# Performance work log

Hardware: AMD Instinct MI355X
Metric: run time of the kernel (lower is better)

## Reference

```python
import math
import jax, jax.numpy as jnp
import numpy as np

NUM_HEADS = 4
HEAD_DIM = 384


def reshape_fortran(x, shape):
    # column-major (Fortran) reshape, matching the torch reverse-permute trick
    x = jnp.transpose(x, tuple(reversed(range(x.ndim))))
    x = x.reshape(tuple(reversed(shape)))
    return jnp.transpose(x, tuple(reversed(range(len(shape)))))


def rel_pos_rotate(data):
    # data: [b, n_heads, L=2M-1, S] -> [b, n_heads, S, S]
    data = jnp.transpose(data, (0, 2, 3, 1))  # [b, d0=L, d1=S, d2=H]
    b, d0, d1, d2 = data.shape
    data = jnp.concatenate([data, jnp.zeros((b, d1, d1, d2), data.dtype)], axis=1)
    data = reshape_fortran(data, (b, (d0 + d1) * d1, 1, d2))
    data = data[:, :(d1 + d0 - 1) * d1]
    data = reshape_fortran(data, (b, d0 + d1 - 1, d1, d2))
    n = d0 // 2
    data = jnp.swapaxes(data[:, n:n + d1], 1, 2)  # [b, d1, d1, d2]
    return jnp.transpose(data, (0, 3, 1, 2))      # [b, H, S, S]


def setup_inputs() -> dict:
    key = jax.random.key(0)
    ks = jax.random.split(key, 5)
    B, S, D = 4, 920, 1536
    M = 920
    return {
        "hidden_states": jax.random.normal(ks[0], (B, S, D), jnp.float32),
        "q_w": jax.random.normal(ks[1], (D, NUM_HEADS * HEAD_DIM), jnp.float32) * 0.02,
        "k_w": jax.random.normal(ks[2], (D, NUM_HEADS * HEAD_DIM), jnp.float32) * 0.02,
        "v_w": jax.random.normal(ks[3], (D, NUM_HEADS * HEAD_DIM), jnp.float32) * 0.02,
        "dist_emb": jax.random.normal(ks[4], (2 * M - 1, HEAD_DIM), jnp.float32) * 0.02,
    }


def reference(hidden_states, q_w, k_w, v_w, dist_emb):
    B, S, D = hidden_states.shape

    def heads(x):  # [B,S,H*hd] -> [B,H,S,hd]
        return jnp.transpose(x.reshape(B, S, NUM_HEADS, HEAD_DIM), (0, 2, 1, 3))

    # query is pre-scaled by 1/sqrt(head_dim), matching the torch code
    q = heads((hidden_states @ q_w) / math.sqrt(HEAD_DIM))
    k = heads(hidden_states @ k_w)
    v = heads(hidden_states @ v_w)

    scores = jnp.einsum("bhqd,bhkd->bhqk", q, k)  # [B,H,S,S]
    # relative position scores: [B,H,L,S] then skew-rotated into [B,H,S,S]
    rel = jnp.einsum("ld,bhsd->bhls", dist_emb, q)
    scores = scores + rel_pos_rotate(rel)

    probs = jax.nn.softmax(scores, axis=-1)
    ctx = jnp.einsum("bhqk,bhkd->bhqd", probs, v)  # [B,H,S,hd]
    ctx = jnp.transpose(ctx, (0, 2, 1, 3)).reshape(B, S, NUM_HEADS * HEAD_DIM)
    return ctx
```

## Files before the change

kernel.cpp:

```cpp
#include <hip/hip_runtime.h>
#include <cstdint>
#include <cstddef>

#define SEQ   920
#define DM    1536
#define DH    384
#define NHD   4
#define NB    4
#define NBH   16
#define MTOK  3680
#define NREL  1839

typedef short          bf16x8 __attribute__((ext_vector_type(8)));
typedef float          f32x4  __attribute__((ext_vector_type(4)));
typedef unsigned short u16x4  __attribute__((ext_vector_type(4)));
typedef unsigned short u16x8  __attribute__((ext_vector_type(8)));

__device__ __forceinline__ unsigned short f2bf(float f){
  union{float f; unsigned u;} v; v.f = f;
  unsigned r = v.u + 0x7FFFu + ((v.u >> 16) & 1u);
  return (unsigned short)(r >> 16);
}
__device__ __forceinline__ float bf2f(unsigned short h){
  union{unsigned u; float f;} v; v.u = ((unsigned)h) << 16;
  return v.f;
}
__device__ __forceinline__ f32x4 mfma_bf16(bf16x8 a, bf16x8 b, f32x4 c){
  return __builtin_amdgcn_mfma_f32_16x16x32_bf16(a, b, c, 0, 0, 0);
}
__device__ __forceinline__ void gload_lds16(const void* g, void* l){
  __builtin_amdgcn_global_load_lds((const __attribute__((address_space(1))) void*)g,
                                   (__attribute__((address_space(3))) void*)l, 16, 0, 0);
}

__global__ __launch_bounds__(256) void k_f2bf(const float* __restrict__ src,
                                              unsigned short* __restrict__ dst, int n){
  int i = (blockIdx.x * 256 + threadIdx.x) * 4;
  int stride = gridDim.x * 256 * 4;
  for(; i + 3 < n; i += stride){
    f32x4 v = *(const f32x4*)(src + i);
    u16x4 o; o.x = f2bf(v.x); o.y = f2bf(v.y); o.z = f2bf(v.z); o.w = f2bf(v.w);
    *(u16x4*)(dst + i) = o;
  }
}

__global__ __launch_bounds__(256) void k_wt3(const float* __restrict__ qw,
                                             const float* __restrict__ kw,
                                             const float* __restrict__ vw,
                                             unsigned short* __restrict__ wt){
  __shared__ float t[32][33];
  const float* w = blockIdx.z == 0 ? qw : (blockIdx.z == 1 ? kw : vw);
  int k0 = blockIdx.x * 32, n0 = blockIdx.y * 32;
  int tx = threadIdx.x, ty = threadIdx.y;
  #pragma unroll
  for(int j = 0; j < 4; j++)
    t[ty*4+j][tx] = w[(size_t)(k0 + ty*4 + j) * DM + n0 + tx];
  __syncthreads();
  #pragma unroll
  for(int j = 0; j < 4; j++)
    wt[(size_t)(blockIdx.z*DM + n0 + ty*4 + j) * DM + k0 + tx] = f2bf(t[tx][ty*4+j]);
}

template<class Epi>
__device__ __forceinline__ void gemm192(const unsigned short* __restrict__ A, int lda, int Amax,
                                        const unsigned short* __restrict__ B, int ldb, int Bmax,
                                        int K, int m0, int n0, Epi epi){
  __shared__ unsigned short As[3*192*64];
  __shared__ unsigned short Bs[3*192*64];
  const int tid = threadIdx.x;
  const int w = tid >> 6, l = tid & 63;
  const int lg = l >> 4, lo = l & 15;
  const int wm = w >> 2, wn = w & 3;

  const char* ga[3]; const char* gb[3];
  #pragma unroll
  for(int r = 0; r < 3; r++){
    int row = r*64 + (tid >> 3);
    int gslot = (tid & 7) ^ (row & 7);
    int ar = m0 + row; ar = ar < Amax ? ar : Amax - 1;
    ga[r] = (const char*)A + (size_t)ar*lda*2 + gslot*16;
    int br = n0 + row; br = br < Bmax ? br : Bmax - 1;
    gb[r] = (const char*)B + (size_t)br*ldb*2 + gslot*16;
  }
  const int ldst = tid * 16;

  auto stage = [&](int kt, int slot){
    size_t koff = (size_t)kt * 128;
    #pragma unroll
    for(int r = 0; r < 3; r++){
      gload_lds16(ga[r] + koff, (char*)As + slot*24576 + r*8192 + ldst);
      gload_lds16(gb[r] + koff, (char*)Bs + slot*24576 + r*8192 + ldst);
    }
  };

  f32x4 acc[6][3] = {};
  const int sw = (lo & 7) << 4;
  const int nk = (2*K + 127) >> 7;
  const int tb = 2*K - (nk - 1)*128;
  const bool keep0 = (lg*16) < tb;
  const bool keep1 = (64 + lg*16) < tb;

  auto compute = [&](int slot, bool last){
    const char* Ab = (const char*)As + slot*24576;
    const char* Bb = (const char*)Bs + slot*24576;
    bf16x8 af[6][2], bf[3][2];
    #pragma unroll
    for(int fi = 0; fi < 6; fi++){
      int row = wm*96 + fi*16 + lo;
      #pragma unroll
      for(int kk = 0; kk < 2; kk++)
        af[fi][kk] = *(const bf16x8*)(Ab + row*128 + ((kk*64 + lg*16) ^ sw));
    }
    #pragma unroll
    for(int fj = 0; fj < 3; fj++){
      int row = wn*48 + fj*16 + lo;
      #pragma unroll
      for(int kk = 0; kk < 2; kk++)
        bf[fj][kk] = *(const bf16x8*)(Bb + row*128 + ((kk*64 + lg*16) ^ sw));
    }
    if(last){
      #pragma unroll
      for(int fi = 0; fi < 6; fi++){
        if(!keep0) af[fi][0] = bf16x8{};
        if(!keep1) af[fi][1] = bf16x8{};
      }
    }
    __builtin_amdgcn_s_setprio(1);
    #pragma unroll
    for(int kk = 0; kk < 2; kk++)
      #pragma unroll
      for(int fi = 0; fi < 6; fi++)
        #pragma unroll
        for(int fj = 0; fj < 3; fj++)
          acc[fi][fj] = mfma_bf16(af[fi][kk], bf[fj][kk], acc[fi][fj]);
    __builtin_amdgcn_s_setprio(0);
  };

  stage(0, 0);
  stage(1, 1);
  int st = 0;
  for(int t = 0; t < nk; t++){
    if(t + 2 < nk){
      int s2 = st + 2 >= 3 ? st - 1 : st + 2;
      stage(t + 2, s2);
      asm volatile("s_waitcnt vmcnt(12)" ::: "memory");
    } else if(t + 1 < nk){
      asm volatile("s_waitcnt vmcnt(6)" ::: "memory");
    } else {
      asm volatile("s_waitcnt vmcnt(0)" ::: "memory");
    }
    __builtin_amdgcn_s_barrier();
    compute(st, t == nk - 1);
    __builtin_amdgcn_s_barrier();
    st = st + 1 >= 3 ? 0 : st + 1;
  }

  #pragma unroll
  for(int fi = 0; fi < 6; fi++)
    #pragma unroll
    for(int fj = 0; fj < 3; fj++){
      int m = m0 + wm*96 + fi*16 + lg*4;
      int n = n0 + wn*48 + fj*16 + lo;
      epi(m, n, acc[fi][fj]);
    }
}

__global__ __launch_bounds__(512) void k_proj(const unsigned short* __restrict__ X,
                                              const unsigned short* __restrict__ Wt,
                                              unsigned short* __restrict__ Qb,
                                              unsigned short* __restrict__ Kb,
                                              unsigned short* __restrict__ Vt){
  int bid = blockIdx.x;
  int wg  = (bid & 7) * 60 + (bid >> 3);
  int m0 = (wg % 20) * 192, n0 = (wg / 20) * 192;
  gemm192(X, DM, MTOK, Wt, DM, 3*DM, DM, m0, n0,
    [=] __device__ (int m, int n, f32x4 v4){
      if(m >= MTOK) return;
      int which = n / DM, r = n % DM, h = r / DH, d = r % DH;
      int b = m / SEQ, s = m % SEQ;
      int bh = b * NHD + h;
      if(which == 2){
        u16x4 o;
        o.x = f2bf(v4.x); o.y = f2bf(v4.y); o.z = f2bf(v4.z); o.w = f2bf(v4.w);
        *(u16x4*)(Vt + ((size_t)bh*DH + d)*SEQ + s) = o;
      } else if(which == 0){
        #pragma unroll
        for(int i = 0; i < 4; i++)
          Qb[((size_t)bh*SEQ + s + i)*DH + d] = f2bf(v4[i] * 0.05103103630798287f);
      } else {
        #pragma unroll
        for(int i = 0; i < 4; i++)
          Kb[((size_t)bh*SEQ + s + i)*DH + d] = f2bf(v4[i]);
      }
    });
}

__global__ __launch_bounds__(512) void k_rel(const unsigned short* __restrict__ Qb,
                                             const unsigned short* __restrict__ E,
                                             unsigned short* __restrict__ relS){
  int m0 = blockIdx.x * 192, n0 = blockIdx.y * 192;
  int s0 = m0 % SEQ;
  int qlo = s0, qhi = s0 + 191;
  if(qhi >= SEQ){ qlo = 0; qhi = SEQ - 1; }
  if(n0 + 191 < 919 - qhi || n0 > 1838 - qlo) return;
  gemm192(Qb, DH, NBH*SEQ, E, DH, NREL, DH, m0, n0,
    [=] __device__ (int m, int n, f32x4 v4){
      #pragma unroll
      for(int i = 0; i < 4; i++){
        int mi = m + i;
        if(mi >= NBH*SEQ) continue;
        int q = mi % SEQ;
        int j = n - 919 + q;
        if(j < 0 || j >= SEQ) continue;
        relS[(size_t)mi*SEQ + j] = f2bf(v4[i]);
      }
    });
}

__global__ __launch_bounds__(512) void k_sgemm(const unsigned short* __restrict__ Qb,
                                               const unsigned short* __restrict__ Kb,
                                               unsigned short* __restrict__ P){
  int id = blockIdx.x;
  int idp = (id & 7) * 50 + (id >> 3);
  int bh = idp / 25, r = idp % 25;
  int m0 = (r % 5) * 192, n0 = (r / 5) * 192;
  const unsigned short* A = Qb + (size_t)bh*SEQ*DH;
  const unsigned short* B = Kb + (size_t)bh*SEQ*DH;
  unsigned short* Pbh = P + (size_t)bh*SEQ*SEQ;
  gemm192(A, DH, SEQ, B, DH, SEQ, DH, m0, n0,
    [=] __device__ (int m, int n, f32x4 v4){
      if(n >= SEQ) return;
      #pragma unroll
      for(int i = 0; i < 4; i++){
        int mi = m + i;
        if(mi >= SEQ) continue;
        size_t off = (size_t)mi*SEQ + n;
        float p = __expf(v4[i] + bf2f(Pbh[off]));
        Pbh[off] = f2bf(p);
      }
    });
}

__global__ __launch_bounds__(256) void k_rowsum(const unsigned short* __restrict__ P,
                                                float* __restrict__ rs){
  int w = threadIdx.x >> 6, l = threadIdx.x & 63;
  #pragma unroll
  for(int r = 0; r < 4; r++){
    int row = blockIdx.x * 16 + w * 4 + r;
    size_t base = (size_t)row * SEQ;
    float s = 0.f;
    for(int c = l; c < 115; c += 64){
      u16x8 v = *(const u16x8*)(P + base + (size_t)c*8);
      #pragma unroll
      for(int j = 0; j < 8; j++) s += bf2f(v[j]);
    }
    s += __shfl_xor(s, 1);  s += __shfl_xor(s, 2);  s += __shfl_xor(s, 4);
    s += __shfl_xor(s, 8);  s += __shfl_xor(s, 16); s += __shfl_xor(s, 32);
    if(l == 0) rs[row] = s;
  }
}

__global__ __launch_bounds__(512) void k_pv(const unsigned short* __restrict__ P,
                                            const unsigned short* __restrict__ Vt,
                                            const float* __restrict__ rs,
                                            float* __restrict__ out){
  int id = blockIdx.x;
  int idp = (id & 7) * 20 + (id >> 3);
  int bh = idp / 10, r = idp % 10;
  int m0 = (r % 5) * 192, n0 = (r / 5) * 192;
  const unsigned short* A = P  + (size_t)bh*SEQ*SEQ;
  const unsigned short* B = Vt + (size_t)bh*DH*SEQ;
  const float* rsb = rs + (size_t)bh*SEQ;
  const int b = bh >> 2, h = bh & 3;
  gemm192(A, SEQ, SEQ, B, SEQ, DH, SEQ, m0, n0,
    [=] __device__ (int m, int n, f32x4 v4){
      #pragma unroll
      for(int i = 0; i < 4; i++){
        int mi = m + i;
        if(mi >= SEQ) continue;
        out[((size_t)(b*SEQ + mi))*DM + h*DH + n] = v4[i] / rsb[mi];
      }
    });
}

extern "C" void kernel_launch(void* const* d_in, const int* in_sizes, int n_in,
                              void* d_out, int out_size, void* d_ws, size_t ws_size,
                              hipStream_t stream){
  const float* X  = (const float*)d_in[0];
  const float* qw = (const float*)d_in[1];
  const float* kw = (const float*)d_in[2];
  const float* vw = (const float*)d_in[3];
  const float* de = (const float*)d_in[4];
  float* out = (float*)d_out;
  char* ws = (char*)d_ws;

  unsigned short* Qb   = (unsigned short*)ws;
  unsigned short* Kb   = (unsigned short*)(ws + 11304960);
  unsigned short* Vt   = (unsigned short*)(ws + 22609920);
  unsigned short* relS = (unsigned short*)(ws + 33914880);
  unsigned short* Eb   = (unsigned short*)(ws + 60999680);
  unsigned short* Xb   = (unsigned short*)(ws + 33914880);
  unsigned short* Wt   = (unsigned short*)(ws + 45219840);
  float*          rsum = (float*)ws;

  k_f2bf<<<dim3(2048), dim3(256), 0, stream>>>(X,  Xb, MTOK*DM);
  k_f2bf<<<dim3(690),  dim3(256), 0, stream>>>(de, Eb, NREL*DH);
  k_wt3<<<dim3(48,48,3), dim3(32,8), 0, stream>>>(qw, kw, vw, Wt);
  k_proj<<<dim3(480), dim3(512), 0, stream>>>(Xb, Wt, Qb, Kb, Vt);
  k_rel<<<dim3(77,10), dim3(512), 0, stream>>>(Qb, Eb, relS);
  k_sgemm<<<dim3(400), dim3(512), 0, stream>>>(Qb, Kb, relS);
  k_rowsum<<<dim3(920), dim3(256), 0, stream>>>(relS, rsum);
  k_pv<<<dim3(160), dim3(512), 0, stream>>>(relS, Vt, rsum, out);
}
```

Before: 230.9 us.

## Interleave GEMM LDS fragment loads and prefetch with MFMA in three phases

Splits each K-tile's compute into three phases of two A-fragments each. Every phase issues one slice of the next-next tile's global-to-LDS prefetch, interleaved with LDS reads and MFMA blocks. The aim is to spread memory traffic across the iteration instead of issuing it all up front, and to lower register pressure from holding all A fragments. It adds extra barriers per iteration and changes the vmcnt wait pattern, which could cost more in synchronization than it saves.

After: 219.7 us. 4.9% less time.

```diff
diff --git a/kernel.cpp b/kernel.cpp
--- a/kernel.cpp
+++ b/kernel.cpp
@@ -84,13 +84,10 @@
   }
   const int ldst = tid * 16;
 
-  auto stage = [&](int kt, int slot){
+  auto stage_pair = [&](int kt, int slot, int r){
     size_t koff = (size_t)kt * 128;
-    #pragma unroll
-    for(int r = 0; r < 3; r++){
-      gload_lds16(ga[r] + koff, (char*)As + slot*24576 + r*8192 + ldst);
-      gload_lds16(gb[r] + koff, (char*)Bs + slot*24576 + r*8192 + ldst);
-    }
+    gload_lds16(ga[r] + koff, (char*)As + slot*24576 + r*8192 + ldst);
+    gload_lds16(gb[r] + koff, (char*)Bs + slot*24576 + r*8192 + ldst);
   };
 
   f32x4 acc[6][3] = {};
@@ -100,58 +97,119 @@
   const bool keep0 = (lg*16) < tb;
   const bool keep1 = (64 + lg*16) < tb;
 
-  auto compute = [&](int slot, bool last){
-    const char* Ab = (const char*)As + slot*24576;
-    const char* Bb = (const char*)Bs + slot*24576;
-    bf16x8 af[6][2], bf[3][2];
-    #pragma unroll
-    for(int fi = 0; fi < 6; fi++){
-      int row = wm*96 + fi*16 + lo;
-      #pragma unroll
-      for(int kk = 0; kk < 2; kk++)
-        af[fi][kk] = *(const bf16x8*)(Ab + row*128 + ((kk*64 + lg*16) ^ sw));
-    }
+  #pragma unroll
+  for(int r = 0; r < 3; r++) stage_pair(0, 0, r);
+  #pragma unroll
+  for(int r = 0; r < 3; r++) stage_pair(1, 1, r);
+  asm volatile("s_waitcnt vmcnt(6)" ::: "memory");
+  __builtin_amdgcn_s_barrier();
+
+  int st = 0;
+  for(int t = 0; t < nk; t++){
+    const bool last = (t == nk - 1);
+    const bool pf = (t + 2 < nk);
+    const int s2 = st + 2 >= 3 ? st - 1 : st + 2;
+    const char* Ab = (const char*)As + st*24576;
+    const char* Bb = (const char*)Bs + st*24576;
+
+    bf16x8 bfr[3][2], afr[2][2];
+
     #pragma unroll
     for(int fj = 0; fj < 3; fj++){
       int row = wn*48 + fj*16 + lo;
       #pragma unroll
       for(int kk = 0; kk < 2; kk++)
-        bf[fj][kk] = *(const bf16x8*)(Bb + row*128 + ((kk*64 + lg*16) ^ sw));
-    }
+        bfr[fj][kk] = *(const bf16x8*)(Bb + row*128 + ((kk*64 + lg*16) ^ sw));
+    }
+    #pragma unroll
+    for(int fi = 0; fi < 2; fi++){
+      int row = wm*96 + fi*16 + lo;
+      #pragma unroll
+      for(int kk = 0; kk < 2; kk++)
+        afr[fi][kk] = *(const bf16x8*)(Ab + row*128 + ((kk*64 + lg*16) ^ sw));
+    }
+    if(pf) stage_pair(t + 2, s2, 0);
     if(last){
       #pragma unroll
-      for(int fi = 0; fi < 6; fi++){
-        if(!keep0) af[fi][0] = bf16x8{};
-        if(!keep1) af[fi][1] = bf16x8{};
-      }
-    }
+      for(int fi = 0; fi < 2; fi++){
+        if(!keep0) afr[fi][0] = bf16x8{};
+        if(!keep1) afr[fi][1] = bf16x8{};
+      }
+    }
+    __builtin_amdgcn_s_barrier();
+    asm volatile("s_waitcnt lgkmcnt(0)" ::: "memory");
     __builtin_amdgcn_s_setprio(1);
     #pragma unroll
     for(int kk = 0; kk < 2; kk++)
       #pragma unroll
-      for(int fi = 0; fi < 6; fi++)
+      for(int fi = 0; fi < 2; fi++)
         #pragma unroll
         for(int fj = 0; fj < 3; fj++)
-          acc[fi][fj] = mfma_bf16(af[fi][kk], bf[fj][kk], acc[fi][fj]);
+          acc[fi][fj] = mfma_bf16(afr[fi][kk], bfr[fj][kk], acc[fi][fj]);
     __builtin_amdgcn_s_setprio(0);
-  };
-
-  stage(0, 0);
-  stage(1, 1);
-  int st = 0;
-  for(int t = 0; t < nk; t++){
-    if(t + 2 < nk){
-      int s2 = st + 2 >= 3 ? st - 1 : st + 2;
-      stage(t + 2, s2);
-      asm volatile("s_waitcnt vmcnt(12)" ::: "memory");
+    __builtin_amdgcn_s_barrier();
+
+    #pragma unroll
+    for(int fi = 0; fi < 2; fi++){
+      int row = wm*96 + (fi + 2)*16 + lo;
+      #pragma unroll
+      for(int kk = 0; kk < 2; kk++)
+        afr[fi][kk] = *(const bf16x8*)(Ab + row*128 + ((kk*64 + lg*16) ^ sw));
+    }
+    if(pf) stage_pair(t + 2, s2, 1);
+    if(last){
+      #pragma unroll
+      for(int fi = 0; fi < 2; fi++){
+        if(!keep0) afr[fi][0] = bf16x8{};
+        if(!keep1) afr[fi][1] = bf16x8{};
+      }
+    }
+    __builtin_amdgcn_s_barrier();
+    asm volatile("s_waitcnt lgkmcnt(0)" ::: "memory");
+    __builtin_amdgcn_s_setprio(1);
+    #pragma unroll
+    for(int kk = 0; kk < 2; kk++)
+      #pragma unroll
+      for(int fi = 0; fi < 2; fi++)
+        #pragma unroll
+        for(int fj = 0; fj < 3; fj++)
+          acc[fi + 2][fj] = mfma_bf16(afr[fi][kk], bfr[fj][kk], acc[fi + 2][fj]);
+    __builtin_amdgcn_s_setprio(0);
+    __builtin_amdgcn_s_barrier();
+
+    #pragma unroll
+    for(int fi = 0; fi < 2; fi++){
+      int row = wm*96 + (fi + 4)*16 + lo;
+      #pragma unroll
+      for(int kk = 0; kk < 2; kk++)
+        afr[fi][kk] = *(const bf16x8*)(Ab + row*128 + ((kk*64 + lg*16) ^ sw));
+    }
+    if(pf){
+      stage_pair(t + 2, s2, 2);
+      asm volatile("s_waitcnt vmcnt(6)" ::: "memory");
     } else if(t + 1 < nk){
-      asm volatile("s_waitcnt vmcnt(6)" ::: "memory");
-    } else {
       asm volatile("s_waitcnt vmcnt(0)" ::: "memory");
     }
-    __builtin_amdgcn_s_barrier();
-    compute(st, t == nk - 1);
-    __builtin_amdgcn_s_barrier();
+    if(last){
+      #pragma unroll
+      for(int fi = 0; fi < 2; fi++){
+        if(!keep0) afr[fi][0] = bf16x8{};
+        if(!keep1) afr[fi][1] = bf16x8{};
+      }
+    }
+    __builtin_amdgcn_s_barrier();
+    asm volatile("s_waitcnt lgkmcnt(0)" ::: "memory");
+    __builtin_amdgcn_s_setprio(1);
+    #pragma unroll
+    for(int kk = 0; kk < 2; kk++)
+      #pragma unroll
+      for(int fi = 0; fi < 2; fi++)
+        #pragma unroll
+        for(int fj = 0; fj < 3; fj++)
+          acc[fi + 4][fj] = mfma_bf16(afr[fi][kk], bfr[fj][kk], acc[fi + 4][fj]);
+    __builtin_amdgcn_s_setprio(0);
+    __builtin_amdgcn_s_barrier();
+
     st = st + 1 >= 3 ? 0 : st + 1;
   }
 
```

## Switch GEMMs to 128x128 tiles with B fragments loaded directly to registers

Applied to the files above, without the earlier changes.

Replaces the shared 192x192 GEMM core, which staged both operands through LDS, with a 128x128 core. Only A is staged through LDS, in a 4-deep ring. B fragments are read straight from global memory into double-buffered registers, which halves LDS traffic and cuts one barrier per k-step. Smaller tiles with launch_bounds(512,4) raise the block count and occupancy, and grids and XCD-aware block mappings are recomputed for every GEMM kernel. The cost is uncoalesced per-lane global reads for B, plus less data reuse per tile.

After: 288.5 us. +24.9%, slower.

```diff
diff --git a/kernel.cpp b/kernel.cpp
--- a/kernel.cpp
+++ b/kernel.cpp
@@ -61,119 +61,125 @@
     wt[(size_t)(blockIdx.z*DM + n0 + ty*4 + j) * DM + k0 + tx] = f2bf(t[tx][ty*4+j]);
 }
 
-template<class Epi>
-__device__ __forceinline__ void gemm192(const unsigned short* __restrict__ A, int lda, int Amax,
+#define GITER(T, BFC, BFN)                                                     \
+  {                                                                            \
+    const int t_ = (T);                                                        \
+    __builtin_amdgcn_s_barrier();                                              \
+    const char* Ab = (const char*)As + (t_ & 3)*16384;                         \
+    bf16x8 af[4][2];                                                           \
+    _Pragma("unroll")                                                          \
+    for(int fi = 0; fi < 4; fi++){                                             \
+      int row = wm*64 + fi*16 + lo;                                            \
+      _Pragma("unroll")                                                        \
+      for(int kk = 0; kk < 2; kk++)                                            \
+        af[fi][kk] = *(const bf16x8*)(Ab + row*128 + ((kk*64 + lg*16) ^ sw));  \
+    }                                                                          \
+    if(t_ + 1 < nk) loadB(t_ + 1, BFN);                                        \
+    if(t_ + 3 < nk) stageA(t_ + 3, (t_ + 3) & 3);                              \
+    if(t_ == nk - 1){                                                          \
+      _Pragma("unroll")                                                        \
+      for(int fi = 0; fi < 4; fi++){                                           \
+        if(!keep0) af[fi][0] = bf16x8{};                                       \
+        if(!keep1) af[fi][1] = bf16x8{};                                       \
+      }                                                                        \
+    }                                                                          \
+    __builtin_amdgcn_s_setprio(1);                                             \
+    _Pragma("unroll")                                                          \
+    for(int kk = 0; kk < 2; kk++)                                              \
+      _Pragma("unroll")                                                        \
+      for(int fi = 0; fi < 4; fi++)                                            \
+        _Pragma("unroll")                                                      \
+        for(int fj = 0; fj < 2; fj++)                                          \
+          acc[fi][fj] = mfma_bf16(af[fi][kk], BFC[fj][kk], acc[fi][fj]);       \
+    __builtin_amdgcn_s_setprio(0);                                             \
+    if(t_ + 2 < nk){ asm volatile("s_waitcnt vmcnt(2)" ::: "memory"); }        \
+    else           { asm volatile("s_waitcnt vmcnt(0)" ::: "memory"); }        \
+  }
+
+template<bool CLAMP_B, class Epi>
+__device__ __forceinline__ void gemm128(const unsigned short* __restrict__ A, int lda, int Amax,
                                         const unsigned short* __restrict__ B, int ldb, int Bmax,
                                         int K, int m0, int n0, Epi epi){
-  __shared__ unsigned short As[3*192*64];
-  __shared__ unsigned short Bs[3*192*64];
+  __shared__ unsigned short As[4*128*64];
   const int tid = threadIdx.x;
   const int w = tid >> 6, l = tid & 63;
   const int lg = l >> 4, lo = l & 15;
   const int wm = w >> 2, wn = w & 3;
 
-  const char* ga[3]; const char* gb[3];
-  #pragma unroll
-  for(int r = 0; r < 3; r++){
+  const char* ga[2];
+  #pragma unroll
+  for(int r = 0; r < 2; r++){
     int row = r*64 + (tid >> 3);
     int gslot = (tid & 7) ^ (row & 7);
     int ar = m0 + row; ar = ar < Amax ? ar : Amax - 1;
     ga[r] = (const char*)A + (size_t)ar*lda*2 + gslot*16;
-    int br = n0 + row; br = br < Bmax ? br : Bmax - 1;
-    gb[r] = (const char*)B + (size_t)br*ldb*2 + gslot*16;
   }
   const int ldst = tid * 16;
 
-  auto stage = [&](int kt, int slot){
+  const char* gbf[2];
+  #pragma unroll
+  for(int fj = 0; fj < 2; fj++){
+    int row = n0 + wn*32 + fj*16 + lo;
+    if(CLAMP_B) row = row < Bmax ? row : Bmax - 1;
+    gbf[fj] = (const char*)B + (size_t)row*ldb*2;
+  }
+
+  auto stageA = [&](int kt, int slot){
     size_t koff = (size_t)kt * 128;
     #pragma unroll
-    for(int r = 0; r < 3; r++){
-      gload_lds16(ga[r] + koff, (char*)As + slot*24576 + r*8192 + ldst);
-      gload_lds16(gb[r] + koff, (char*)Bs + slot*24576 + r*8192 + ldst);
-    }
+    for(int r = 0; r < 2; r++)
+      gload_lds16(ga[r] + koff, (char*)As + slot*16384 + r*8192 + ldst);
   };
-
-  f32x4 acc[6][3] = {};
+  auto loadB = [&](int kt, bf16x8 (&bf)[2][2]){
+    size_t koff = (size_t)kt * 128;
+    #pragma unroll
+    for(int fj = 0; fj < 2; fj++)
+      #pragma unroll
+      for(int kk = 0; kk < 2; kk++)
+        bf[fj][kk] = *(const bf16x8*)(gbf[fj] + koff + kk*64 + lg*16);
+  };
+
+  f32x4 acc[4][2] = {};
   const int sw = (lo & 7) << 4;
   const int nk = (2*K + 127) >> 7;
   const int tb = 2*K - (nk - 1)*128;
   const bool keep0 = (lg*16) < tb;
   const bool keep1 = (64 + lg*16) < tb;
 
-  auto compute = [&](int slot, bool last){
-    const char* Ab = (const char*)As + slot*24576;
-    const char* Bb = (const char*)Bs + slot*24576;
-    bf16x8 af[6][2], bf[3][2];
+  bf16x8 bfA[2][2], bfB[2][2];
+  stageA(0, 0);
+  loadB(0, bfA);
+  stageA(1, 1);
+  stageA(2, 2);
+  asm volatile("s_waitcnt vmcnt(4)" ::: "memory");
+
+  int t = 0;
+  for(; t + 1 < nk; t += 2){
+    GITER(t,     bfA, bfB);
+    GITER(t + 1, bfB, bfA);
+  }
+  if(t < nk) GITER(t, bfA, bfB);
+
+  #pragma unroll
+  for(int fi = 0; fi < 4; fi++)
     #pragma unroll
-    for(int fi = 0; fi < 6; fi++){
-      int row = wm*96 + fi*16 + lo;
-      #pragma unroll
-      for(int kk = 0; kk < 2; kk++)
-        af[fi][kk] = *(const bf16x8*)(Ab + row*128 + ((kk*64 + lg*16) ^ sw));
-    }
-    #pragma unroll
-    for(int fj = 0; fj < 3; fj++){
-      int row = wn*48 + fj*16 + lo;
-      #pragma unroll
-      for(int kk = 0; kk < 2; kk++)
-        bf[fj][kk] = *(const bf16x8*)(Bb + row*128 + ((kk*64 + lg*16) ^ sw));
-    }
-    if(last){
-      #pragma unroll
-      for(int fi = 0; fi < 6; fi++){
-        if(!keep0) af[fi][0] = bf16x8{};
-        if(!keep1) af[fi][1] = bf16x8{};
-      }
-    }
-    __builtin_amdgcn_s_setprio(1);
-    #pragma unroll
-    for(int kk = 0; kk < 2; kk++)
-      #pragma unroll
-      for(int fi = 0; fi < 6; fi++)
-        #pragma unroll
-        for(int fj = 0; fj < 3; fj++)
-          acc[fi][fj] = mfma_bf16(af[fi][kk], bf[fj][kk], acc[fi][fj]);
-    __builtin_amdgcn_s_setprio(0);
-  };
-
-  stage(0, 0);
-  stage(1, 1);
-  int st = 0;
-  for(int t = 0; t < nk; t++){
-    if(t + 2 < nk){
-      int s2 = st + 2 >= 3 ? st - 1 : st + 2;
-      stage(t + 2, s2);
-      asm volatile("s_waitcnt vmcnt(12)" ::: "memory");
-    } else if(t + 1 < nk){
-      asm volatile("s_waitcnt vmcnt(6)" ::: "memory");
-    } else {
-      asm volatile("s_waitcnt vmcnt(0)" ::: "memory");
-    }
-    __builtin_amdgcn_s_barrier();
-    compute(st, t == nk - 1);
-    __builtin_amdgcn_s_barrier();
-    st = st + 1 >= 3 ? 0 : st + 1;
-  }
-
-  #pragma unroll
-  for(int fi = 0; fi < 6; fi++)
-    #pragma unroll
-    for(int fj = 0; fj < 3; fj++){
-      int m = m0 + wm*96 + fi*16 + lg*4;
-      int n = n0 + wn*48 + fj*16 + lo;
+    for(int fj = 0; fj < 2; fj++){
+      int m = m0 + wm*64 + fi*16 + lg*4;
+      int n = n0 + wn*32 + fj*16 + lo;
       epi(m, n, acc[fi][fj]);
     }
 }
 
-__global__ __launch_bounds__(512) void k_proj(const unsigned short* __restrict__ X,
-                                              const unsigned short* __restrict__ Wt,
-                                              unsigned short* __restrict__ Qb,
-                                              unsigned short* __restrict__ Kb,
-                                              unsigned short* __restrict__ Vt){
+__global__ __launch_bounds__(512, 4) void k_proj(const unsigned short* __restrict__ X,
+                                                 const unsigned short* __restrict__ Wt,
+                                                 unsigned short* __restrict__ Qb,
+                                                 unsigned short* __restrict__ Kb,
+                                                 unsigned short* __restrict__ Vt){
   int bid = blockIdx.x;
-  int wg  = (bid & 7) * 60 + (bid >> 3);
-  int m0 = (wg % 20) * 192, n0 = (wg / 20) * 192;
-  gemm192(X, DM, MTOK, Wt, DM, 3*DM, DM, m0, n0,
+  int xcd = bid & 7;
+  int wg = (xcd < 4 ? xcd*131 : 4*131 + (xcd - 4)*130) + (bid >> 3);
+  int m0 = (wg % 29) * 128, n0 = (wg / 29) * 128;
+  gemm128<false>(X, DM, MTOK, Wt, DM, 3*DM, DM, m0, n0,
     [=] __device__ (int m, int n, f32x4 v4){
       if(m >= MTOK) return;
       int which = n / DM, r = n % DM, h = r / DH, d = r % DH;
@@ -195,20 +201,19 @@
     });
 }
 
-__global__ __launch_bounds__(512) void k_rel(const unsigned short* __restrict__ Qb,
-                                             const unsigned short* __restrict__ E,
-                                             unsigned short* __restrict__ relS){
-  int m0 = blockIdx.x * 192, n0 = blockIdx.y * 192;
+__global__ __launch_bounds__(512, 4) void k_rel(const unsigned short* __restrict__ Qb,
+                                                const unsigned short* __restrict__ E,
+                                                unsigned short* __restrict__ relS){
+  int m0 = blockIdx.x * 128, n0 = blockIdx.y * 128;
   int s0 = m0 % SEQ;
-  int qlo = s0, qhi = s0 + 191;
+  int qlo = s0, qhi = s0 + 127;
   if(qhi >= SEQ){ qlo = 0; qhi = SEQ - 1; }
-  if(n0 + 191 < 919 - qhi || n0 > 1838 - qlo) return;
-  gemm192(Qb, DH, NBH*SEQ, E, DH, NREL, DH, m0, n0,
+  if(n0 + 127 < 919 - qhi || n0 > 1838 - qlo) return;
+  gemm128<true>(Qb, DH, NBH*SEQ, E, DH, NREL, DH, m0, n0,
     [=] __device__ (int m, int n, f32x4 v4){
       #pragma unroll
       for(int i = 0; i < 4; i++){
         int mi = m + i;
-        if(mi >= NBH*SEQ) continue;
         int q = mi % SEQ;
         int j = n - 919 + q;
         if(j < 0 || j >= SEQ) continue;
@@ -217,17 +222,17 @@
     });
 }
 
-__global__ __launch_bounds__(512) void k_sgemm(const unsigned short* __restrict__ Qb,
-                                               const unsigned short* __restrict__ Kb,
-                                               unsigned short* __restrict__ P){
-  int id = blockIdx.x;
-  int idp = (id & 7) * 50 + (id >> 3);
-  int bh = idp / 25, r = idp % 25;
-  int m0 = (r % 5) * 192, n0 = (r / 5) * 192;
+__global__ __launch_bounds__(512, 4) void k_sgemm(const unsigned short* __restrict__ Qb,
+                                                  const unsigned short* __restrict__ Kb,
+                                                  unsigned short* __restrict__ P){
+  int bid = blockIdx.x;
+  int wg = (bid & 7) * 128 + (bid >> 3);
+  int bh = wg >> 6, r = wg & 63;
+  int m0 = (r & 7) * 128, n0 = (r >> 3) * 128;
   const unsigned short* A = Qb + (size_t)bh*SEQ*DH;
   const unsigned short* B = Kb + (size_t)bh*SEQ*DH;
   unsigned short* Pbh = P + (size_t)bh*SEQ*SEQ;
-  gemm192(A, DH, SEQ, B, DH, SEQ, DH, m0, n0,
+  gemm128<true>(A, DH, SEQ, B, DH, SEQ, DH, m0, n0,
     [=] __device__ (int m, int n, f32x4 v4){
       if(n >= SEQ) return;
       #pragma unroll
@@ -260,19 +265,19 @@
   }
 }
 
-__global__ __launch_bounds__(512) void k_pv(const unsigned short* __restrict__ P,
-                                            const unsigned short* __restrict__ Vt,
-                                            const float* __restrict__ rs,
-                                            float* __restrict__ out){
-  int id = blockIdx.x;
-  int idp = (id & 7) * 20 + (id >> 3);
-  int bh = idp / 10, r = idp % 10;
-  int m0 = (r % 5) * 192, n0 = (r / 5) * 192;
+__global__ __launch_bounds__(512, 4) void k_pv(const unsigned short* __restrict__ P,
+                                               const unsigned short* __restrict__ Vt,
+                                               const float* __restrict__ rs,
+                                               float* __restrict__ out){
+  int bid = blockIdx.x;
+  int wg = (bid & 7) * 48 + (bid >> 3);
+  int bh = wg / 24, r = wg % 24;
+  int m0 = (r / 3) * 128, n0 = (r % 3) * 128;
   const unsigned short* A = P  + (size_t)bh*SEQ*SEQ;
   const unsigned short* B = Vt + (size_t)bh*DH*SEQ;
   const float* rsb = rs + (size_t)bh*SEQ;
   const int b = bh >> 2, h = bh & 3;
-  gemm192(A, SEQ, SEQ, B, SEQ, DH, SEQ, m0, n0,
+  gemm128<false>(A, SEQ, SEQ, B, SEQ, DH, SEQ, m0, n0,
     [=] __device__ (int m, int n, f32x4 v4){
       #pragma unroll
       for(int i = 0; i < 4; i++){
@@ -306,9 +311,9 @@
   k_f2bf<<<dim3(2048), dim3(256), 0, stream>>>(X,  Xb, MTOK*DM);
   k_f2bf<<<dim3(690),  dim3(256), 0, stream>>>(de, Eb, NREL*DH);
   k_wt3<<<dim3(48,48,3), dim3(32,8), 0, stream>>>(qw, kw, vw, Wt);
-  k_proj<<<dim3(480), dim3(512), 0, stream>>>(Xb, Wt, Qb, Kb, Vt);
-  k_rel<<<dim3(77,10), dim3(512), 0, stream>>>(Qb, Eb, relS);
-  k_sgemm<<<dim3(400), dim3(512), 0, stream>>>(Qb, Kb, relS);
+  k_proj<<<dim3(1044), dim3(512), 0, stream>>>(Xb, Wt, Qb, Kb, Vt);
+  k_rel<<<dim3(115,15), dim3(512), 0, stream>>>(Qb, Eb, relS);
+  k_sgemm<<<dim3(1024), dim3(512), 0, stream>>>(Qb, Kb, relS);
   k_rowsum<<<dim3(920), dim3(256), 0, stream>>>(relS, rsum);
-  k_pv<<<dim3(160), dim3(512), 0, stream>>>(relS, Vt, rsum, out);
-}
+  k_pv<<<dim3(384), dim3(512), 0, stream>>>(relS, Vt, rsum, out);
+}
```
